# Kernel tuning notes

Measured on AMD Instinct MI355X. Metric: run time of the kernel, lower is better.

## Reference

```python
import jax, jax.numpy as jnp
import numpy as np

B, S, D = 4, 4096, 1024
H, F = 16, 256
HD = D // H  # 64


def setup_inputs() -> dict:
    key = jax.random.key(0)
    ks = jax.random.split(key, 10)
    scale = 1.0 / np.sqrt(D)
    x = jax.random.normal(ks[0], (B, S, D), dtype=jnp.float32)
    Wq = jax.random.normal(ks[1], (D, D), dtype=jnp.float32) * scale
    bq = jnp.zeros((D,), dtype=jnp.float32)
    Wk = jax.random.normal(ks[2], (D, D), dtype=jnp.float32) * scale
    bk = jnp.zeros((D,), dtype=jnp.float32)
    Wv = jax.random.normal(ks[3], (D, D), dtype=jnp.float32) * scale
    bv = jnp.zeros((D,), dtype=jnp.float32)
    Wo = jax.random.normal(ks[4], (D, D), dtype=jnp.float32) * scale
    bo = jnp.zeros((D,), dtype=jnp.float32)
    rf = jax.random.normal(ks[5], (H, HD, F), dtype=jnp.float32) / np.sqrt(F)
    return {"x": x, "Wq": Wq, "bq": bq, "Wk": Wk, "bk": bk,
            "Wv": Wv, "bv": bv, "Wo": Wo, "bo": bo, "rf": rf}


def _heads(y):
    # [B,S,D] -> [B,H,S,HD]
    return y.reshape(B, S, H, HD).transpose(0, 2, 1, 3)


def reference(x, Wq, bq, Wk, bk, Wv, bv, Wo, bo, rf):
    q = _heads(x @ Wq.T + bq)
    k = _heads(x @ Wk.T + bk)
    v = _heads(x @ Wv.T + bv)
    # positive feature maps: softplus(random projection)
    q_prime = jax.nn.softplus(jnp.einsum('bhsd,hdf->bhsf', q, rf))
    k_prime = jax.nn.softplus(jnp.einsum('bhsd,hdf->bhsf', k, rf))
    kv = jnp.einsum('bhsf,bhsd->bhfd', k_prime, v)          # [B,H,F,HD]
    k_sum = k_prime.sum(axis=2)                              # [B,H,F]
    qkv = jnp.einsum('bhsf,bhfd->bhsd', q_prime, kv)        # [B,H,S,HD]
    denom = jnp.einsum('bhsf,bhf->bhs', q_prime, k_sum) + 1e-8
    out = qkv / denom[..., None]
    out = out.transpose(0, 2, 1, 3).reshape(B, S, D)
    return out @ Wo.T + bo
```

## Files before the change

kernel.cpp:

```cpp
#include <hip/hip_runtime.h>
#include <hip/hip_bf16.h>
#include <math.h>

#define Bb 4
#define Ss 4096
#define Dd 1024
#define Hh 16
#define Ff 256
#define HDd 64
#define Mm (Bb*Ss)

typedef unsigned int u32;
typedef unsigned short u16;

typedef __attribute__((ext_vector_type(8))) short bf16x8;
typedef __attribute__((ext_vector_type(4))) float f32x4;

__device__ __forceinline__ float bflo(u32 u){ union{u32 i; float f;} c; c.i = u << 16; return c.f; }
__device__ __forceinline__ float bfhi(u32 u){ union{u32 i; float f;} c; c.i = u & 0xffff0000u; return c.f; }
__device__ __forceinline__ u16 f2b(float f){
  union{float f; u32 i;} c; c.f = f;
  u32 x = c.i;
  return (u16)((x + 0x7fffu + ((x >> 16) & 1u)) >> 16);
}
__device__ __forceinline__ u32 pk2(float lo, float hi){
  union { __hip_bfloat162 h; u32 u; } c;
  c.h = __float22bfloat162_rn(make_float2(lo, hi));
  return c.u;
}
__device__ __forceinline__ float sfast(float x){
  return fmaxf(x, 0.f) + __logf(1.f + __expf(-fabsf(x)));
}
__device__ __forceinline__ void gload_lds16(const u16* g, u16* l){
  __builtin_amdgcn_global_load_lds(
      (const __attribute__((address_space(1))) void*)g,
      (__attribute__((address_space(3))) void*)l, 16, 0, 0);
}

__global__ void cvt_bf16(const float* __restrict__ in, u16* __restrict__ out, int n)
{
  int i = (blockIdx.x * 256 + threadIdx.x) * 8;
  if (i >= n) return;
  float4 a = *reinterpret_cast<const float4*>(in + i);
  float4 b = *reinterpret_cast<const float4*>(in + i + 4);
  *reinterpret_cast<uint4*>(out + i) =
      make_uint4(pk2(a.x, a.y), pk2(a.z, a.w), pk2(b.x, b.y), pk2(b.z, b.w));
}

__global__ void zero_f32(float* __restrict__ p, int n)
{
  int i = blockIdx.x * 256 + threadIdx.x;
  if (i < n) p[i] = 0.f;
}

template<typename OT, bool BROW>
__global__ __launch_bounds__(256, 2) void mfma_gemm_bt(
    const u16* __restrict__ A, const u16* __restrict__ W,
    const float* __restrict__ bias, OT* __restrict__ C,
    int M, int N, int K)
{
  __shared__ __align__(16) u16 As[128 * 32];
  __shared__ __align__(16) u16 Bs[128 * 32];

  const int tid = threadIdx.x;
  const int wave = tid >> 6, lane = tid & 63;
  const int quad = lane >> 4, lm = lane & 15;
  const int wm = (wave >> 1) * 64, wn = (wave & 1) * 64;
  const int m0 = blockIdx.x * 128, n0 = blockIdx.y * 128;

  f32x4 acc[4][4] = {};

  for (int k0 = 0; k0 < K; k0 += 32) {
#pragma unroll
    for (int j = 0; j < 2; j++) {
      const int c = wave * 128 + j * 64 + lane;
      const int r = c >> 2, cg = c & 3;
      u16* ldsA = &As[(wave * 128 + j * 64) * 8];
      u16* ldsB = &Bs[(wave * 128 + j * 64) * 8];
      gload_lds16(A + (size_t)(m0 + r) * K + k0 + cg * 8, ldsA);
      gload_lds16(W + (size_t)(n0 + r) * K + k0 + cg * 8, ldsB);
    }
    __syncthreads();

    bf16x8 af[4], bf[4];
#pragma unroll
    for (int mi = 0; mi < 4; mi++)
      af[mi] = *reinterpret_cast<const bf16x8*>(&As[(wm + mi * 16 + lm) * 32 + quad * 8]);
#pragma unroll
    for (int ni = 0; ni < 4; ni++)
      bf[ni] = *reinterpret_cast<const bf16x8*>(&Bs[(wn + ni * 16 + lm) * 32 + quad * 8]);
#pragma unroll
    for (int mi = 0; mi < 4; mi++)
#pragma unroll
      for (int ni = 0; ni < 4; ni++)
        acc[mi][ni] = __builtin_amdgcn_mfma_f32_16x16x32_bf16(af[mi], bf[ni], acc[mi][ni], 0, 0, 0);
    __syncthreads();
  }

#pragma unroll
  for (int mi = 0; mi < 4; mi++)
#pragma unroll
    for (int ni = 0; ni < 4; ni++) {
      const int n = n0 + wn + ni * 16 + lm;
      const float bvn = BROW ? 0.f : bias[n];
#pragma unroll
      for (int r = 0; r < 4; r++) {
        const int m = m0 + wm + mi * 16 + quad * 4 + r;
        const float val = acc[mi][ni][r] + (BROW ? bias[m] : bvn);
        if constexpr (sizeof(OT) == 2) ((u16*)C)[(size_t)m * N + n] = f2b(val);
        else                           ((float*)C)[(size_t)m * N + n] = val;
      }
    }
}

__global__ void rf_transpose(const float* __restrict__ rf, float* __restrict__ rft)
{
  const int h = blockIdx.x, d = blockIdx.y, f = threadIdx.x;
  rft[((size_t)h * Ff + f) * HDd + d] = rf[((size_t)(h * HDd + d)) * Ff + f];
}

#define NSPLIT 16
#define SCHUNKS (Ss / NSPLIT / 64)

__global__ __launch_bounds__(256, 2) void kv_fused(
    const u16* __restrict__ Km, const u16* __restrict__ Vt,
    const float* __restrict__ rft, float* __restrict__ kv, float* __restrict__ ksum)
{
  __shared__ __align__(16) u16 KS[64 * 64];
  __shared__ __align__(16) u16 VS[64 * 64];
  __shared__ __align__(16) u16 PT[4][64 * 64];

  const int bh = blockIdx.x;
  const int b = bh >> 4, h = bh & 15;
  const int s0 = blockIdx.y * (Ss / NSPLIT);
  const int tid = threadIdx.x;
  const int wave = tid >> 6, lane = tid & 63;
  const int quad = lane >> 4, lm = lane & 15;
  const int F0 = wave * 64;

  bf16x8 bfr[4][2];
  {
    const float* rh = rft + (size_t)h * Ff * HDd;
#pragma unroll
    for (int ni = 0; ni < 4; ni++) {
      const float* rrow = rh + (size_t)(F0 + ni * 16 + lm) * HDd;
#pragma unroll
      for (int ks = 0; ks < 2; ks++) {
        float4 a = *reinterpret_cast<const float4*>(rrow + ks * 32 + quad * 8);
        float4 e = *reinterpret_cast<const float4*>(rrow + ks * 32 + quad * 8 + 4);
        union { u32 w[4]; bf16x8 v; } u;
        u.w[0] = pk2(a.x, a.y); u.w[1] = pk2(a.z, a.w);
        u.w[2] = pk2(e.x, e.y); u.w[3] = pk2(e.z, e.w);
        bfr[ni][ks] = u.v;
      }
    }
  }

  const int j0 = wave * 64 + lane, j1 = j0 + 256;
  const int r0 = j0 >> 3, c0 = (j0 & 7) ^ (r0 & 7);
  const int r1 = j1 >> 3, c1 = (j1 & 7) ^ (r1 & 7);

  f32x4 kvacc[4][4] = {};
  float kss[4] = {0.f, 0.f, 0.f, 0.f};

#pragma unroll 1
  for (int ch = 0; ch < SCHUNKS; ch++) {
    const int sc = s0 + ch * 64;
    gload_lds16(Km + (size_t)(b * Ss + sc + r0) * Dd + h * 64 + c0 * 8, &KS[(wave * 64) * 8]);
    gload_lds16(Km + (size_t)(b * Ss + sc + r1) * Dd + h * 64 + c1 * 8, &KS[(wave * 64 + 256) * 8]);
    gload_lds16(Vt + (size_t)(h * 64 + r0) * Mm + b * Ss + sc + c0 * 8, &VS[(wave * 64) * 8]);
    gload_lds16(Vt + (size_t)(h * 64 + r1) * Mm + b * Ss + sc + c1 * 8, &VS[(wave * 64 + 256) * 8]);
    __syncthreads();

#pragma unroll
    for (int mi = 0; mi < 4; mi++) {
      const int row = mi * 16 + lm;
      f32x4 pmi[4] = {};
#pragma unroll
      for (int ks2 = 0; ks2 < 2; ks2++) {
        bf16x8 af = *reinterpret_cast<const bf16x8*>(
            (const char*)KS + row * 128 + (((ks2 * 4 + quad) ^ (row & 7)) * 16));
#pragma unroll
        for (int ni = 0; ni < 4; ni++)
          pmi[ni] = __builtin_amdgcn_mfma_f32_16x16x32_bf16(af, bfr[ni][ks2], pmi[ni], 0, 0, 0);
      }
#pragma unroll
      for (int ni = 0; ni < 4; ni++) {
        float v0 = sfast(pmi[ni][0]);
        float v1 = sfast(pmi[ni][1]);
        float v2 = sfast(pmi[ni][2]);
        float v3 = sfast(pmi[ni][3]);
        kss[ni] += (v0 + v1) + (v2 + v3);
        int frow = ni * 16 + lm;
        int off = (frow * 128 + mi * 32 + quad * 8) ^ ((frow & 7) << 4);
        *reinterpret_cast<uint2*>((char*)&PT[wave][0] + off) =
            make_uint2(pk2(v0, v1), pk2(v2, v3));
      }
    }

#pragma unroll
    for (int ks2 = 0; ks2 < 2; ks2++) {
      bf16x8 a2[4], b2[4];
#pragma unroll
      for (int mi = 0; mi < 4; mi++) {
        int row = mi * 16 + lm;
        a2[mi] = *reinterpret_cast<const bf16x8*>(
            (char*)&PT[wave][0] + row * 128 + (((ks2 * 4 + quad) ^ (row & 7)) * 16));
      }
#pragma unroll
      for (int ni = 0; ni < 4; ni++) {
        int row = ni * 16 + lm;
        b2[ni] = *reinterpret_cast<const bf16x8*>(
            (const char*)VS + row * 128 + (((ks2 * 4 + quad) ^ (row & 7)) * 16));
      }
#pragma unroll
      for (int mi = 0; mi < 4; mi++)
#pragma unroll
        for (int ni = 0; ni < 4; ni++)
          kvacc[mi][ni] = __builtin_amdgcn_mfma_f32_16x16x32_bf16(a2[mi], b2[ni], kvacc[mi][ni], 0, 0, 0);
    }
    __syncthreads();
  }

  float* kvp = kv + (size_t)bh * Ff * HDd;
#pragma unroll
  for (int mi = 0; mi < 4; mi++)
#pragma unroll
    for (int ni = 0; ni < 4; ni++)
#pragma unroll
      for (int rr = 0; rr < 4; rr++) {
        int f = F0 + mi * 16 + quad * 4 + rr;
        int d = ni * 16 + lm;
        atomicAdd(kvp + (size_t)f * HDd + d, kvacc[mi][ni][rr]);
      }
#pragma unroll
  for (int ni = 0; ni < 4; ni++) {
    float v = kss[ni];
    v += __shfl_xor(v, 16, 64);
    v += __shfl_xor(v, 32, 64);
    if (quad == 0) atomicAdd(ksum + (size_t)bh * Ff + F0 + ni * 16 + lm, v);
  }
}

__global__ void kvt_cvt(const float* __restrict__ kv, u16* __restrict__ kvtb)
{
  const int bh = blockIdx.x;
  const int d = threadIdx.x & 63, fg = threadIdx.x >> 6;
  const float* src = kv + (size_t)bh * Ff * HDd + d;
  u32* dst = reinterpret_cast<u32*>(kvtb + (size_t)bh * HDd * Ff + (size_t)d * Ff + fg * 64);
#pragma unroll
  for (int j = 0; j < 32; j++) {
    float v0 = src[(size_t)(fg * 64 + 2 * j) * HDd];
    float v1 = src[(size_t)(fg * 64 + 2 * j + 1) * HDd];
    dst[j] = pk2(v0, v1);
  }
}

#define ASPLIT 16
#define ACHUNKS (Ss / ASPLIT / 64)

__global__ __launch_bounds__(256, 2) void attn_fused(
    const u16* __restrict__ Qm, const float* __restrict__ rft,
    const u16* __restrict__ kvtb, const float* __restrict__ ksum,
    u16* __restrict__ attnb)
{
  __shared__ __align__(16) u16 P4[4][64 * 64];
  __shared__ __align__(16) float den4[64][4];

  const int bh = blockIdx.x;
  const int b = bh >> 4, h = bh & 15;
  const int s0 = blockIdx.y * (Ss / ASPLIT);
  const int tid = threadIdx.x;
  const int wave = tid >> 6, lane = tid & 63;
  const int quad = lane >> 4, lm = lane & 15;
  const int F0 = wave * 64;

  bf16x8 bfr[4][2];
  {
    const float* rh = rft + (size_t)h * Ff * HDd;
#pragma unroll
    for (int ni = 0; ni < 4; ni++) {
      const float* rrow = rh + (size_t)(F0 + ni * 16 + lm) * HDd;
#pragma unroll
      for (int ks = 0; ks < 2; ks++) {
        float4 a = *reinterpret_cast<const float4*>(rrow + ks * 32 + quad * 8);
        float4 e = *reinterpret_cast<const float4*>(rrow + ks * 32 + quad * 8 + 4);
        union { u32 w[4]; bf16x8 v; } u;
        u.w[0] = pk2(a.x, a.y); u.w[1] = pk2(a.z, a.w);
        u.w[2] = pk2(e.x, e.y); u.w[3] = pk2(e.z, e.w);
        bfr[ni][ks] = u.v;
      }
    }
  }
  bf16x8 b2r[4][2];
  {
    const u16* kb = kvtb + (size_t)bh * HDd * Ff + (size_t)(wave * 16 + lm) * Ff;
#pragma unroll
    for (int fb = 0; fb < 4; fb++)
#pragma unroll
      for (int k2 = 0; k2 < 2; k2++)
        b2r[fb][k2] = *reinterpret_cast<const bf16x8*>(kb + fb * 64 + k2 * 32 + quad * 8);
  }
  float ksv[4];
#pragma unroll
  for (int ni = 0; ni < 4; ni++)
    ksv[ni] = ksum[(size_t)bh * Ff + F0 + ni * 16 + lm];

  for (int ch = 0; ch < ACHUNKS; ch++) {
    const int sc0 = s0 + ch * 64;

    bf16x8 af[4][2];
#pragma unroll
    for (int mi = 0; mi < 4; mi++) {
      const u16* qrow = Qm + (size_t)(b * Ss + sc0 + mi * 16 + lm) * Dd + h * 64;
#pragma unroll
      for (int ks = 0; ks < 2; ks++)
        af[mi][ks] = *reinterpret_cast<const bf16x8*>(qrow + ks * 32 + quad * 8);
    }
    f32x4 p[4][4] = {};
#pragma unroll
    for (int ks = 0; ks < 2; ks++)
#pragma unroll
      for (int mi = 0; mi < 4; mi++)
#pragma unroll
        for (int ni = 0; ni < 4; ni++)
          p[mi][ni] = __builtin_amdgcn_mfma_f32_16x16x32_bf16(af[mi][ks], bfr[ni][ks], p[mi][ni], 0, 0, 0);

#pragma unroll
    for (int mi = 0; mi < 4; mi++) {
      const int sbase = mi * 16 + quad * 4;
      float dd[4] = {0.f, 0.f, 0.f, 0.f};
#pragma unroll
      for (int ni = 0; ni < 4; ni++) {
        u32 pk01 = pk2(sfast(p[mi][ni][0]), sfast(p[mi][ni][1]));
        u32 pk23 = pk2(sfast(p[mi][ni][2]), sfast(p[mi][ni][3]));
        dd[0] += bflo(pk01) * ksv[ni];
        dd[1] += bfhi(pk01) * ksv[ni];
        dd[2] += bflo(pk23) * ksv[ni];
        dd[3] += bfhi(pk23) * ksv[ni];
        u32 ob01 = (u32)__shfl_xor((int)pk01, 1, 64);
        u32 ob23 = (u32)__shfl_xor((int)pk23, 1, 64);
        const int odd = lm & 1;
        u32 w_a = odd ? ((ob23 & 0xffffu) | (pk23 << 16))
                      : ((pk01 & 0xffffu) | (ob01 << 16));
        u32 w_b = odd ? ((ob23 >> 16)     | (pk23 & 0xffff0000u))
                      : ((pk01 >> 16)     | (ob01 & 0xffff0000u));
        const int row_a = sbase + (odd ? 2 : 0);
        const int row_b = sbase + (odd ? 3 : 1);
        const int fpb = ni * 16 + (lm & ~1);
        const int cc = fpb >> 3;
        const int bib = (fpb & 7) * 2;
        *reinterpret_cast<u32*>((char*)&P4[wave][0] + row_a * 128 + ((cc ^ (row_a & 7)) << 4) + bib) = w_a;
        *reinterpret_cast<u32*>((char*)&P4[wave][0] + row_b * 128 + ((cc ^ (row_b & 7)) << 4) + bib) = w_b;
      }
#pragma unroll
      for (int r = 0; r < 4; r++) {
        float v = dd[r];
        v += __shfl_xor(v, 1, 64);
        v += __shfl_xor(v, 2, 64);
        v += __shfl_xor(v, 4, 64);
        v += __shfl_xor(v, 8, 64);
        if (lm == 0) den4[sbase + r][wave] = v;
      }
    }
    __syncthreads();

    f32x4 acc2[4] = {};
#pragma unroll
    for (int fb = 0; fb < 4; fb++)
#pragma unroll
      for (int k2 = 0; k2 < 2; k2++) {
        bf16x8 af2[4];
#pragma unroll
        for (int mi = 0; mi < 4; mi++) {
          int row = mi * 16 + lm;
          af2[mi] = *reinterpret_cast<const bf16x8*>(
              (char*)&P4[fb][0] + row * 128 + (((k2 * 4 + quad) ^ (row & 7)) << 4));
        }
#pragma unroll
        for (int mi = 0; mi < 4; mi++)
          acc2[mi] = __builtin_amdgcn_mfma_f32_16x16x32_bf16(af2[mi], b2r[fb][k2], acc2[mi], 0, 0, 0);
      }

#pragma unroll
    for (int mi = 0; mi < 4; mi++) {
#pragma unroll
      for (int r = 0; r < 4; r++) {
        const int s = mi * 16 + quad * 4 + r;
        float4 dv = *reinterpret_cast<const float4*>(&den4[s][0]);
        const float inv = 1.f / ((dv.x + dv.y) + (dv.z + dv.w) + 1e-8f);
        attnb[(size_t)(b * Ss + sc0 + s) * Dd + h * 64 + wave * 16 + lm] =
            f2b(acc2[mi][r] * inv);
      }
    }
    __syncthreads();
  }
}

extern "C" void kernel_launch(void* const* d_in, const int* in_sizes, int n_in,
                              void* d_out, int out_size, void* d_ws, size_t ws_size,
                              hipStream_t stream)
{
  const float* x  = (const float*)d_in[0];
  const float* Wq = (const float*)d_in[1];
  const float* bq = (const float*)d_in[2];
  const float* Wk = (const float*)d_in[3];
  const float* bk = (const float*)d_in[4];
  const float* Wv = (const float*)d_in[5];
  const float* bv = (const float*)d_in[6];
  const float* Wo = (const float*)d_in[7];
  const float* bo = (const float*)d_in[8];
  const float* rf = (const float*)d_in[9];

  char* w = (char*)d_ws;
  u16* xb = (u16*)w;        w += (size_t)Mm * Dd * 2;
  u16* q  = (u16*)w;        w += (size_t)Mm * Dd * 2;
  u16* k  = (u16*)w;        w += (size_t)Mm * Dd * 2;
  u16* vt = (u16*)w;        w += (size_t)Mm * Dd * 2;
  u16* wqb = (u16*)w;       w += (size_t)Dd * Dd * 2;
  u16* wkb = (u16*)w;       w += (size_t)Dd * Dd * 2;
  u16* wvb = (u16*)w;       w += (size_t)Dd * Dd * 2;
  u16* wob = (u16*)w;       w += (size_t)Dd * Dd * 2;
  float* kv = (float*)w;    w += (size_t)(Bb * Hh) * Ff * HDd * 4;
  float* ks = (float*)w;    w += (size_t)(Bb * Hh) * Ff * 4;
  float* rft = (float*)w;   w += (size_t)Hh * Ff * HDd * 4;
  u16* kvtb = wqb;

  cvt_bf16<<<(Mm * Dd / 8 + 255) / 256, 256, 0, stream>>>(x, xb, Mm * Dd);
  cvt_bf16<<<(Dd * Dd / 8 + 255) / 256, 256, 0, stream>>>(Wq, wqb, Dd * Dd);
  cvt_bf16<<<(Dd * Dd / 8 + 255) / 256, 256, 0, stream>>>(Wk, wkb, Dd * Dd);
  cvt_bf16<<<(Dd * Dd / 8 + 255) / 256, 256, 0, stream>>>(Wv, wvb, Dd * Dd);
  cvt_bf16<<<(Dd * Dd / 8 + 255) / 256, 256, 0, stream>>>(Wo, wob, Dd * Dd);

  const int nz = (Bb * Hh) * Ff * HDd + (Bb * Hh) * Ff;
  zero_f32<<<(nz + 255) / 256, 256, 0, stream>>>(kv, nz);
  rf_transpose<<<dim3(Hh, HDd), 256, 0, stream>>>(rf, rft);

  const dim3 gg(Mm / 128, Dd / 128);
  mfma_gemm_bt<u16, false><<<gg, 256, 0, stream>>>(xb, wqb, bq, q, Mm, Dd, Dd);
  mfma_gemm_bt<u16, false><<<gg, 256, 0, stream>>>(xb, wkb, bk, k, Mm, Dd, Dd);
  const dim3 gv(Dd / 128, Mm / 128);
  mfma_gemm_bt<u16, true><<<gv, 256, 0, stream>>>(wvb, xb, bv, vt, Dd, Mm, Dd);

  kv_fused<<<dim3(Bb * Hh, NSPLIT), 256, 0, stream>>>(k, vt, rft, kv, ks);

  kvt_cvt<<<Bb * Hh, 256, 0, stream>>>(kv, kvtb);

  attn_fused<<<dim3(Bb * Hh, ASPLIT), 256, 0, stream>>>(q, rft, kvtb, ks, xb);

  mfma_gemm_bt<float, false><<<gg, 256, 0, stream>>>(xb, wob, bo, (float*)d_out, Mm, Dd, Dd);
}
```

Measured before the change: 505.8 us.

## Double GEMM K-tile with XOR-swizzled LDS, batch weight conversion, tidy attention stores

The GEMM K-step goes from 32 to 64 per LDS stage, with an XOR swizzle on the 16-byte column chunks. This halves the number of barriers per K and is meant to avoid LDS bank conflicts. The four weight-conversion launches are merged into one 2D launch. In the attention kernel, the P-tile LDS offsets are hoisted out of the chunk loop and the bf16 repacking now uses v_perm, and the output stores pack two values with one conversion. The larger LDS tiles (32KB per block) may reduce occupancy.

```diff
diff --git a/kernel.cpp b/kernel.cpp
--- a/kernel.cpp
+++ b/kernel.cpp
@@ -47,6 +47,19 @@
       make_uint4(pk2(a.x, a.y), pk2(a.z, a.w), pk2(b.x, b.y), pk2(b.z, b.w));
 }
 
+__global__ void cvt_w4(const float* __restrict__ w0, const float* __restrict__ w1,
+                       const float* __restrict__ w2, const float* __restrict__ w3,
+                       u16* __restrict__ out)
+{
+  const int y = blockIdx.y;
+  const float* in = (y == 0) ? w0 : (y == 1) ? w1 : (y == 2) ? w2 : w3;
+  int i = (blockIdx.x * 256 + threadIdx.x) * 8;
+  float4 a = *reinterpret_cast<const float4*>(in + i);
+  float4 b = *reinterpret_cast<const float4*>(in + i + 4);
+  *reinterpret_cast<uint4*>(out + (size_t)y * Dd * Dd + i) =
+      make_uint4(pk2(a.x, a.y), pk2(a.z, a.w), pk2(b.x, b.y), pk2(b.z, b.w));
+}
+
 __global__ void zero_f32(float* __restrict__ p, int n)
 {
   int i = blockIdx.x * 256 + threadIdx.x;
@@ -59,8 +72,8 @@
     const float* __restrict__ bias, OT* __restrict__ C,
     int M, int N, int K)
 {
-  __shared__ __align__(16) u16 As[128 * 32];
-  __shared__ __align__(16) u16 Bs[128 * 32];
+  __shared__ __align__(16) u16 As[128 * 64];
+  __shared__ __align__(16) u16 Bs[128 * 64];
 
   const int tid = threadIdx.x;
   const int wave = tid >> 6, lane = tid & 63;
@@ -68,32 +81,47 @@
   const int wm = (wave >> 1) * 64, wn = (wave & 1) * 64;
   const int m0 = blockIdx.x * 128, n0 = blockIdx.y * 128;
 
+  int rr[4], cc4[4];
+#pragma unroll
+  for (int i = 0; i < 4; i++) {
+    const int j = wave * 64 + i * 256 + lane;
+    rr[i] = j >> 3;
+    cc4[i] = (j & 7) ^ (rr[i] & 7);
+  }
+
   f32x4 acc[4][4] = {};
 
-  for (int k0 = 0; k0 < K; k0 += 32) {
-#pragma unroll
-    for (int j = 0; j < 2; j++) {
-      const int c = wave * 128 + j * 64 + lane;
-      const int r = c >> 2, cg = c & 3;
-      u16* ldsA = &As[(wave * 128 + j * 64) * 8];
-      u16* ldsB = &Bs[(wave * 128 + j * 64) * 8];
-      gload_lds16(A + (size_t)(m0 + r) * K + k0 + cg * 8, ldsA);
-      gload_lds16(W + (size_t)(n0 + r) * K + k0 + cg * 8, ldsB);
+  for (int k0 = 0; k0 < K; k0 += 64) {
+#pragma unroll
+    for (int i = 0; i < 4; i++) {
+      u16* ldsA = &As[(wave * 64 + i * 256) * 8];
+      u16* ldsB = &Bs[(wave * 64 + i * 256) * 8];
+      gload_lds16(A + (size_t)(m0 + rr[i]) * K + k0 + cc4[i] * 8, ldsA);
+      gload_lds16(W + (size_t)(n0 + rr[i]) * K + k0 + cc4[i] * 8, ldsB);
     }
     __syncthreads();
 
-    bf16x8 af[4], bf[4];
-#pragma unroll
-    for (int mi = 0; mi < 4; mi++)
-      af[mi] = *reinterpret_cast<const bf16x8*>(&As[(wm + mi * 16 + lm) * 32 + quad * 8]);
-#pragma unroll
-    for (int ni = 0; ni < 4; ni++)
-      bf[ni] = *reinterpret_cast<const bf16x8*>(&Bs[(wn + ni * 16 + lm) * 32 + quad * 8]);
-#pragma unroll
-    for (int mi = 0; mi < 4; mi++)
-#pragma unroll
-      for (int ni = 0; ni < 4; ni++)
-        acc[mi][ni] = __builtin_amdgcn_mfma_f32_16x16x32_bf16(af[mi], bf[ni], acc[mi][ni], 0, 0, 0);
+#pragma unroll
+    for (int ks2 = 0; ks2 < 2; ks2++) {
+      bf16x8 af[4], bf[4];
+#pragma unroll
+      for (int mi = 0; mi < 4; mi++) {
+        const int row = wm + mi * 16 + lm;
+        af[mi] = *reinterpret_cast<const bf16x8*>(
+            &As[row * 64 + (((ks2 * 4 + quad) ^ (row & 7)) * 8)]);
+      }
+#pragma unroll
+      for (int ni = 0; ni < 4; ni++) {
+        const int row = wn + ni * 16 + lm;
+        bf[ni] = *reinterpret_cast<const bf16x8*>(
+            &Bs[row * 64 + (((ks2 * 4 + quad) ^ (row & 7)) * 8)]);
+      }
+#pragma unroll
+      for (int mi = 0; mi < 4; mi++)
+#pragma unroll
+        for (int ni = 0; ni < 4; ni++)
+          acc[mi][ni] = __builtin_amdgcn_mfma_f32_16x16x32_bf16(af[mi], bf[ni], acc[mi][ni], 0, 0, 0);
+    }
     __syncthreads();
   }
 
@@ -103,12 +131,21 @@
     for (int ni = 0; ni < 4; ni++) {
       const int n = n0 + wn + ni * 16 + lm;
       const float bvn = BROW ? 0.f : bias[n];
-#pragma unroll
-      for (int r = 0; r < 4; r++) {
-        const int m = m0 + wm + mi * 16 + quad * 4 + r;
-        const float val = acc[mi][ni][r] + (BROW ? bias[m] : bvn);
-        if constexpr (sizeof(OT) == 2) ((u16*)C)[(size_t)m * N + n] = f2b(val);
-        else                           ((float*)C)[(size_t)m * N + n] = val;
+      const int mb = m0 + wm + mi * 16 + quad * 4;
+      float v[4];
+#pragma unroll
+      for (int r = 0; r < 4; r++)
+        v[r] = acc[mi][ni][r] + (BROW ? bias[mb + r] : bvn);
+      if constexpr (sizeof(OT) == 2) {
+        const u32 w01 = pk2(v[0], v[1]), w23 = pk2(v[2], v[3]);
+        ((u16*)C)[(size_t)(mb + 0) * N + n] = (u16)w01;
+        ((u16*)C)[(size_t)(mb + 1) * N + n] = (u16)(w01 >> 16);
+        ((u16*)C)[(size_t)(mb + 2) * N + n] = (u16)w23;
+        ((u16*)C)[(size_t)(mb + 3) * N + n] = (u16)(w23 >> 16);
+      } else {
+#pragma unroll
+        for (int r = 0; r < 4; r++)
+          ((float*)C)[(size_t)(mb + r) * N + n] = v[r];
       }
     }
 }
@@ -228,10 +265,10 @@
 #pragma unroll
     for (int ni = 0; ni < 4; ni++)
 #pragma unroll
-      for (int rr = 0; rr < 4; rr++) {
-        int f = F0 + mi * 16 + quad * 4 + rr;
+      for (int rr2 = 0; rr2 < 4; rr2++) {
+        int f = F0 + mi * 16 + quad * 4 + rr2;
         int d = ni * 16 + lm;
-        atomicAdd(kvp + (size_t)f * HDd + d, kvacc[mi][ni][rr]);
+        atomicAdd(kvp + (size_t)f * HDd + d, kvacc[mi][ni][rr2]);
       }
 #pragma unroll
   for (int ni = 0; ni < 4; ni++) {
@@ -305,6 +342,21 @@
 #pragma unroll
   for (int ni = 0; ni < 4; ni++)
     ksv[ni] = ksum[(size_t)bh * Ff + F0 + ni * 16 + lm];
+
+  const int odd = lm & 1;
+  u32 pOffA[4], pOffB[4];
+  char* const ptb = (char*)&P4[wave][0];
+  {
+    const int ra = quad * 4 + (odd ? 2 : 0);
+    const int rb = quad * 4 + (odd ? 3 : 1);
+#pragma unroll
+    for (int ni = 0; ni < 4; ni++) {
+      const int fpb = ni * 16 + (lm & ~1);
+      const int cc = fpb >> 3, bib = (fpb & 7) * 2;
+      pOffA[ni] = ra * 128 + ((cc ^ (ra & 7)) << 4) + bib;
+      pOffB[ni] = rb * 128 + ((cc ^ (rb & 7)) << 4) + bib;
+    }
+  }
 
   for (int ch = 0; ch < ACHUNKS; ch++) {
     const int sc0 = s0 + ch * 64;
@@ -340,18 +392,12 @@
         dd[3] += bfhi(pk23) * ksv[ni];
         u32 ob01 = (u32)__shfl_xor((int)pk01, 1, 64);
         u32 ob23 = (u32)__shfl_xor((int)pk23, 1, 64);
-        const int odd = lm & 1;
-        u32 w_a = odd ? ((ob23 & 0xffffu) | (pk23 << 16))
-                      : ((pk01 & 0xffffu) | (ob01 << 16));
-        u32 w_b = odd ? ((ob23 >> 16)     | (pk23 & 0xffff0000u))
-                      : ((pk01 >> 16)     | (ob01 & 0xffff0000u));
-        const int row_a = sbase + (odd ? 2 : 0);
-        const int row_b = sbase + (odd ? 3 : 1);
-        const int fpb = ni * 16 + (lm & ~1);
-        const int cc = fpb >> 3;
-        const int bib = (fpb & 7) * 2;
-        *reinterpret_cast<u32*>((char*)&P4[wave][0] + row_a * 128 + ((cc ^ (row_a & 7)) << 4) + bib) = w_a;
-        *reinterpret_cast<u32*>((char*)&P4[wave][0] + row_b * 128 + ((cc ^ (row_b & 7)) << 4) + bib) = w_b;
+        u32 s0v = odd ? ob23 : pk01;
+        u32 s1v = odd ? pk23 : ob01;
+        u32 w_a = __builtin_amdgcn_perm(s1v, s0v, 0x05040100u);
+        u32 w_b = __builtin_amdgcn_perm(s1v, s0v, 0x07060302u);
+        *reinterpret_cast<u32*>(ptb + pOffA[ni] + mi * 2048) = w_a;
+        *reinterpret_cast<u32*>(ptb + pOffB[ni] + mi * 2048) = w_b;
       }
 #pragma unroll
       for (int r = 0; r < 4; r++) {
@@ -384,14 +430,20 @@
 
 #pragma unroll
     for (int mi = 0; mi < 4; mi++) {
+      float o[4];
 #pragma unroll
       for (int r = 0; r < 4; r++) {
         const int s = mi * 16 + quad * 4 + r;
         float4 dv = *reinterpret_cast<const float4*>(&den4[s][0]);
         const float inv = 1.f / ((dv.x + dv.y) + (dv.z + dv.w) + 1e-8f);
-        attnb[(size_t)(b * Ss + sc0 + s) * Dd + h * 64 + wave * 16 + lm] =
-            f2b(acc2[mi][r] * inv);
-      }
+        o[r] = acc2[mi][r] * inv;
+      }
+      const u32 w01 = pk2(o[0], o[1]), w23 = pk2(o[2], o[3]);
+      const size_t ob = (size_t)(b * Ss + sc0 + mi * 16 + quad * 4) * Dd + h * 64 + wave * 16 + lm;
+      attnb[ob]          = (u16)w01;
+      attnb[ob + Dd]     = (u16)(w01 >> 16);
+      attnb[ob + 2 * Dd] = (u16)w23;
+      attnb[ob + 3 * Dd] = (u16)(w23 >> 16);
     }
     __syncthreads();
   }
@@ -427,10 +479,7 @@
   u16* kvtb = wqb;
 
   cvt_bf16<<<(Mm * Dd / 8 + 255) / 256, 256, 0, stream>>>(x, xb, Mm * Dd);
-  cvt_bf16<<<(Dd * Dd / 8 + 255) / 256, 256, 0, stream>>>(Wq, wqb, Dd * Dd);
-  cvt_bf16<<<(Dd * Dd / 8 + 255) / 256, 256, 0, stream>>>(Wk, wkb, Dd * Dd);
-  cvt_bf16<<<(Dd * Dd / 8 + 255) / 256, 256, 0, stream>>>(Wv, wvb, Dd * Dd);
-  cvt_bf16<<<(Dd * Dd / 8 + 255) / 256, 256, 0, stream>>>(Wo, wob, Dd * Dd);
+  cvt_w4<<<dim3(Dd * Dd / 8 / 256, 4), 256, 0, stream>>>(Wq, Wk, Wv, Wo, wqb);
 
   const int nz = (Bb * Hh) * Ff * HDd + (Bb * Hh) * Ff;
   zero_f32<<<(nz + 255) / 256, 256, 0, stream>>>(kv, nz);
```

New measurement: 499.4 us. No clear change (-1.3%).
